# Performance work log

Hardware: AMD Instinct MI355X
Metric: run time of the kernel (lower is better)

The kernel has to match this reference:

```python
import jax, jax.numpy as jnp
import numpy as np

B, T, U = 8192, 1024, 1024  # batch, token_length, units

def _glorot(key, shape):
    fan_in, fan_out = shape
    limit = np.sqrt(6.0 / (fan_in + fan_out))
    return jax.random.uniform(key, shape, jnp.float32, -limit, limit)

def setup_inputs() -> dict:
    key = jax.random.key(0)
    ks = jax.random.split(key, 7)
    x = jax.random.normal(ks[0], (B, T), jnp.float32)
    h = jax.random.normal(ks[1], (B, U), jnp.float32)
    c = jax.random.normal(ks[2], (B, U), jnp.float32)
    W_i = _glorot(ks[3], (T + U, U))
    W_f = _glorot(ks[4], (T + U, U))
    W_g = _glorot(ks[5], (T + U, U))
    W_o = _glorot(ks[6], (T + U, U))
    b_i = jnp.zeros((U,), jnp.float32)
    b_f = jnp.zeros((U,), jnp.float32)
    b_g = jnp.zeros((U,), jnp.float32)
    b_o = jnp.zeros((U,), jnp.float32)
    return {"x": x, "h": h, "c": c, "W_i": W_i, "W_f": W_f, "W_g": W_g,
            "W_o": W_o, "b_i": b_i, "b_f": b_f, "b_g": b_g, "b_o": b_o}

def reference(x, h, c, W_i, W_f, W_g, W_o, b_i, b_f, b_g, b_o):
    x_h = jnp.concatenate([x, h], axis=-1)  # [B, T+U]
    # fused wide GEMM over the four gates
    W = jnp.concatenate([W_i, W_f, W_g, W_o], axis=1)  # [T+U, 4U]
    b = jnp.concatenate([b_i, b_f, b_g, b_o], axis=0)  # [4U]
    z = x_h @ W + b  # [B, 4U]
    zi, zf, zg, zo = jnp.split(z, 4, axis=-1)
    i = jax.nn.sigmoid(zi)
    f = jax.nn.sigmoid(zf)
    g = jnp.tanh(zg)
    o = jax.nn.sigmoid(zo)
    c_new = f * c + i * g
    h_new = o * jnp.tanh(c_new)
    return (h_new, c_new)
```

## Files before the change

### kernel.cpp

```cpp
#include <hip/hip_runtime.h>
#include <hip/hip_bf16.h>
#include <stdint.h>

#define NKT 32
#define BK 64
#define BM 128
#define GCOLS 128

typedef float f32x4 __attribute__((ext_vector_type(4)));
typedef __bf16 bf16x8 __attribute__((ext_vector_type(8)));

static __device__ __forceinline__ void gll16(const void* g, void* l) {
  __builtin_amdgcn_global_load_lds(
      (const __attribute__((address_space(1))) void*)g,
      (__attribute__((address_space(3))) void*)l, 16, 0, 0);
}

static __device__ __forceinline__ unsigned short f2bf(float f) {
  __hip_bfloat16 h = __float2bfloat16(f);
  union { __hip_bfloat16 h; unsigned short u; } v{h};
  return v.u;
}

__global__ void pack_a(const float* __restrict__ x, const float* __restrict__ h,
                       char* __restrict__ Ap) {
  int t   = blockIdx.x * 256 + threadIdx.x;
  int row = t >> 8;
  int cg  = t & 255;
  int kt  = cg >> 3;
  int c   = cg & 7;
  int rb  = row >> 7;
  int r   = row & 127;
  int gk  = kt * 64 + c * 8;
  const float* src = (gk < 1024) ? (x + (size_t)row * 1024 + gk)
                                 : (h + (size_t)row * 1024 + (gk - 1024));
  float4 lo = *(const float4*)(src);
  float4 hi = *(const float4*)(src + 4);
  unsigned short o[8] = { f2bf(lo.x), f2bf(lo.y), f2bf(lo.z), f2bf(lo.w),
                          f2bf(hi.x), f2bf(hi.y), f2bf(hi.z), f2bf(hi.w) };
  size_t tile = ((size_t)rb * NKT + kt) * 16384;
  char* dst = Ap + tile + (size_t)r * 128 + ((c ^ (r & 7)) * 16);
  *(int4*)dst = *(const int4*)o;
}

__global__ void pack_w(const float* __restrict__ Wi, const float* __restrict__ Wf,
                       const float* __restrict__ Wg, const float* __restrict__ Wo,
                       char* __restrict__ Wp) {
  __shared__ float tile[64][33];
  int kt = blockIdx.x, cb = blockIdx.y, g = blockIdx.z;
  const float* W = (g == 0) ? Wi : (g == 1) ? Wf : (g == 2) ? Wg : Wo;
  int t = threadIdx.x;
  {
    int k  = t >> 2;
    int co = (t & 3) * 8;
    const float* s = W + ((size_t)(kt * 64 + k)) * 1024 + cb * 32 + co;
    float4 lo = *(const float4*)s;
    float4 hi = *(const float4*)(s + 4);
    tile[k][co + 0] = lo.x; tile[k][co + 1] = lo.y; tile[k][co + 2] = lo.z; tile[k][co + 3] = lo.w;
    tile[k][co + 4] = hi.x; tile[k][co + 5] = hi.y; tile[k][co + 6] = hi.z; tile[k][co + 7] = hi.w;
  }
  __syncthreads();
  {
    int gcl = t >> 3;
    int cch = t & 7;
    int gc  = g * 32 + gcl;
    unsigned short o[8];
#pragma unroll
    for (int j = 0; j < 8; ++j) o[j] = f2bf(tile[cch * 8 + j][gcl]);
    size_t tb = ((size_t)cb * NKT + kt) * 16384;
    char* dst = Wp + tb + (size_t)gc * 128 + ((cch ^ (gc & 7)) * 16);
    *(int4*)dst = *(const int4*)o;
  }
}

__global__ __launch_bounds__(256, 2)
void lstm_gemm(const char* __restrict__ Ap, const char* __restrict__ Wp,
               const float* __restrict__ c_in,
               const float* __restrict__ b_i, const float* __restrict__ b_f,
               const float* __restrict__ b_g, const float* __restrict__ b_o,
               float* __restrict__ out) {
  __shared__ __align__(128) char smem[32768];
  char* sA = smem;
  char* sB = smem + 16384;

  int cb = blockIdx.x, rb = blockIdx.y;
  int tid = threadIdx.x;
  int w = tid >> 6, lane = tid & 63;
  int l15 = lane & 15, lq = lane >> 4;

  f32x4 acc[2][8] = {};

  const char* aBase = Ap + ((size_t)rb * NKT) * 16384;
  const char* bBase = Wp + ((size_t)cb * NKT) * 16384;

  int rA0 = w * 32 + l15;
  int rA1 = rA0 + 16;
  int aSwz0 = (rA0 & 7) << 4, aSwz1 = (rA1 & 7) << 4;

  for (int kt = 0; kt < NKT; ++kt) {
    const char* at = aBase + (size_t)kt * 16384;
    const char* bt = bBase + (size_t)kt * 16384;
#pragma unroll
    for (int i = 0; i < 4; ++i) {
      int ldso = (i * 4 + w) * 1024;
      int off  = ldso + lane * 16;
      gll16(at + off, sA + ldso);
      gll16(bt + off, sB + ldso);
    }
    __syncthreads();
#pragma unroll
    for (int ks = 0; ks < 2; ++ks) {
      int kterm = ks * 64 + lq * 16;
      bf16x8 a0 = *(const bf16x8*)(sA + rA0 * 128 + (kterm ^ aSwz0));
      bf16x8 a1 = *(const bf16x8*)(sA + rA1 * 128 + (kterm ^ aSwz1));
#pragma unroll
      for (int n = 0; n < 8; ++n) {
        int gc = n * 16 + l15;
        bf16x8 b = *(const bf16x8*)(sB + gc * 128 + (kterm ^ ((gc & 7) << 4)));
        acc[0][n] = __builtin_amdgcn_mfma_f32_16x16x32_bf16(a0, b, acc[0][n], 0, 0, 0);
        acc[1][n] = __builtin_amdgcn_mfma_f32_16x16x32_bf16(a1, b, acc[1][n], 0, 0, 0);
      }
    }
    __syncthreads();
  }

  const size_t HN = (size_t)8192 * 1024;
#pragma unroll
  for (int ci = 0; ci < 2; ++ci) {
    int col = cb * 32 + ci * 16 + l15;
    float bi = b_i[col], bf = b_f[col], bg = b_g[col], bo = b_o[col];
#pragma unroll
    for (int m = 0; m < 2; ++m) {
      f32x4 zi = acc[m][0 + ci], zf = acc[m][2 + ci];
      f32x4 zg = acc[m][4 + ci], zo = acc[m][6 + ci];
      int row0 = rb * 128 + w * 32 + m * 16 + lq * 4;
#pragma unroll
      for (int r = 0; r < 4; ++r) {
        int row = row0 + r;
        float xi = zi[r] + bi, xf = zf[r] + bf, xg = zg[r] + bg, xo = zo[r] + bo;
        float iv = 1.f / (1.f + __expf(-xi));
        float fv = 1.f / (1.f + __expf(-xf));
        float gv = 1.f - 2.f / (__expf(2.f * xg) + 1.f);
        float ov = 1.f / (1.f + __expf(-xo));
        float cv = c_in[(size_t)row * 1024 + col];
        float cn = fv * cv + iv * gv;
        float tc = 1.f - 2.f / (__expf(2.f * cn) + 1.f);
        out[(size_t)row * 1024 + col]      = ov * tc;
        out[HN + (size_t)row * 1024 + col] = cn;
      }
    }
  }
}

extern "C" void kernel_launch(void* const* d_in, const int* in_sizes, int n_in,
                              void* d_out, int out_size, void* d_ws, size_t ws_size,
                              hipStream_t stream) {
  const float* x  = (const float*)d_in[0];
  const float* h  = (const float*)d_in[1];
  const float* c  = (const float*)d_in[2];
  const float* Wi = (const float*)d_in[3];
  const float* Wf = (const float*)d_in[4];
  const float* Wg = (const float*)d_in[5];
  const float* Wo = (const float*)d_in[6];
  const float* bi = (const float*)d_in[7];
  const float* bf = (const float*)d_in[8];
  const float* bg = (const float*)d_in[9];
  const float* bo = (const float*)d_in[10];

  char* Ap = (char*)d_ws;
  char* Wp = Ap + (size_t)8192 * 2048 * 2;
  float* out = (float*)d_out;

  hipLaunchKernelGGL(pack_a, dim3(8192), dim3(256), 0, stream, x, h, Ap);
  hipLaunchKernelGGL(pack_w, dim3(32, 32, 4), dim3(256), 0, stream, Wi, Wf, Wg, Wo, Wp);
  hipLaunchKernelGGL(lstm_gemm, dim3(32, 64), dim3(256), 0, stream,
                     Ap, Wp, c, bi, bf, bg, bo, out);
}
```

Before: 318.9 us.

## Restructure LSTM GEMM into 256x256 tiles with 4-stage async LDS pipeline

Repacks A and W into 32-wide K tiles with a new XOR swizzle, and raises the GEMM block tile to 256x256 with 512 threads (8 waves in a 2x4 grid). It adds a 4-buffer global_load_lds pipeline that prefetches three tiles ahead, interleaved with MFMA bursts under s_setprio, plus a swizzled block-to-tile mapping for L2 locality. The goal is to hide global load latency and raise arithmetic intensity per LDS byte over the old single-buffered 128x128 loop. In exchange it uses 128KB of LDS and many accumulator registers, which limits occupancy, and the manual vmcnt waits are fragile.

```diff
diff --git a/kernel.cpp b/kernel.cpp
--- a/kernel.cpp
+++ b/kernel.cpp
@@ -2,10 +2,6 @@
 #include <hip/hip_bf16.h>
 #include <stdint.h>
 
-#define NKT 32
-#define BK 64
-#define BM 128
-#define GCOLS 128
 
 typedef float f32x4 __attribute__((ext_vector_type(4)));
 typedef __bf16 bf16x8 __attribute__((ext_vector_type(8)));
@@ -17,137 +13,165 @@
 }
 
 static __device__ __forceinline__ unsigned short f2bf(float f) {
-  __hip_bfloat16 h = __float2bfloat16(f);
-  union { __hip_bfloat16 h; unsigned short u; } v{h};
+  union { __hip_bfloat16 h; unsigned short u; } v{__float2bfloat16(f)};
   return v.u;
 }
 
 __global__ void pack_a(const float* __restrict__ x, const float* __restrict__ h,
                        char* __restrict__ Ap) {
-  int t   = blockIdx.x * 256 + threadIdx.x;
-  int row = t >> 8;
-  int cg  = t & 255;
-  int kt  = cg >> 3;
-  int c   = cg & 7;
-  int rb  = row >> 7;
-  int r   = row & 127;
-  int gk  = kt * 64 + c * 8;
+  int row = blockIdx.x;
+  int c8  = threadIdx.x;
+  int kt  = c8 >> 2, kq = c8 & 3;
+  int gk  = c8 * 8;
   const float* src = (gk < 1024) ? (x + (size_t)row * 1024 + gk)
                                  : (h + (size_t)row * 1024 + (gk - 1024));
-  float4 lo = *(const float4*)(src);
+  float4 lo = *(const float4*)src;
   float4 hi = *(const float4*)(src + 4);
-  unsigned short o[8] = { f2bf(lo.x), f2bf(lo.y), f2bf(lo.z), f2bf(lo.w),
-                          f2bf(hi.x), f2bf(hi.y), f2bf(hi.z), f2bf(hi.w) };
-  size_t tile = ((size_t)rb * NKT + kt) * 16384;
-  char* dst = Ap + tile + (size_t)r * 128 + ((c ^ (r & 7)) * 16);
+  __attribute__((aligned(16))) unsigned short o[8] = {
+      f2bf(lo.x), f2bf(lo.y), f2bf(lo.z), f2bf(lo.w),
+      f2bf(hi.x), f2bf(hi.y), f2bf(hi.z), f2bf(hi.w) };
+  int r = row & 255;
+  int chunk = r * 4 + (kq ^ ((r >> 1) & 3));
+  char* dst = Ap + ((size_t)((row >> 8) * 64 + kt)) * 16384 + chunk * 16;
   *(int4*)dst = *(const int4*)o;
 }
 
 __global__ void pack_w(const float* __restrict__ Wi, const float* __restrict__ Wf,
                        const float* __restrict__ Wg, const float* __restrict__ Wo,
                        char* __restrict__ Wp) {
-  __shared__ float tile[64][33];
-  int kt = blockIdx.x, cb = blockIdx.y, g = blockIdx.z;
+  __shared__ float tile[32][65];
+  int kt = blockIdx.x;
+  int cbo = blockIdx.y;
+  int g = blockIdx.z;
   const float* W = (g == 0) ? Wi : (g == 1) ? Wf : (g == 2) ? Wg : Wo;
   int t = threadIdx.x;
   {
-    int k  = t >> 2;
-    int co = (t & 3) * 8;
-    const float* s = W + ((size_t)(kt * 64 + k)) * 1024 + cb * 32 + co;
+    int k  = t >> 3;
+    int c8 = (t & 7) * 8;
+    const float* s = W + (size_t)(kt * 32 + k) * 1024 + cbo * 64 + c8;
     float4 lo = *(const float4*)s;
     float4 hi = *(const float4*)(s + 4);
-    tile[k][co + 0] = lo.x; tile[k][co + 1] = lo.y; tile[k][co + 2] = lo.z; tile[k][co + 3] = lo.w;
-    tile[k][co + 4] = hi.x; tile[k][co + 5] = hi.y; tile[k][co + 6] = hi.z; tile[k][co + 7] = hi.w;
+    tile[k][c8 + 0] = lo.x; tile[k][c8 + 1] = lo.y; tile[k][c8 + 2] = lo.z; tile[k][c8 + 3] = lo.w;
+    tile[k][c8 + 4] = hi.x; tile[k][c8 + 5] = hi.y; tile[k][c8 + 6] = hi.z; tile[k][c8 + 7] = hi.w;
   }
   __syncthreads();
   {
-    int gcl = t >> 3;
-    int cch = t & 7;
-    int gc  = g * 32 + gcl;
-    unsigned short o[8];
-#pragma unroll
-    for (int j = 0; j < 8; ++j) o[j] = f2bf(tile[cch * 8 + j][gcl]);
-    size_t tb = ((size_t)cb * NKT + kt) * 16384;
-    char* dst = Wp + tb + (size_t)gc * 128 + ((cch ^ (gc & 7)) * 16);
+    int cl = t >> 2;
+    int kq = t & 3;
+    __attribute__((aligned(16))) unsigned short o[8];
+#pragma unroll
+    for (int j = 0; j < 8; ++j) o[j] = f2bf(tile[kq * 8 + j][cl]);
+    int gc = ((cl >> 4) & 3) * 64 + g * 16 + (cl & 15);
+    int chunk = gc * 4 + (kq ^ ((gc >> 1) & 3));
+    char* dst = Wp + ((size_t)(cbo * 64 + kt)) * 16384 + chunk * 16;
     *(int4*)dst = *(const int4*)o;
   }
 }
 
-__global__ __launch_bounds__(256, 2)
+__global__ __launch_bounds__(512, 2)
 void lstm_gemm(const char* __restrict__ Ap, const char* __restrict__ Wp,
                const float* __restrict__ c_in,
                const float* __restrict__ b_i, const float* __restrict__ b_f,
                const float* __restrict__ b_g, const float* __restrict__ b_o,
                float* __restrict__ out) {
-  __shared__ __align__(128) char smem[32768];
-  char* sA = smem;
-  char* sB = smem + 16384;
-
-  int cb = blockIdx.x, rb = blockIdx.y;
+  __shared__ __align__(128) char smem[131072];
+
   int tid = threadIdx.x;
-  int w = tid >> 6, lane = tid & 63;
-  int l15 = lane & 15, lq = lane >> 4;
-
-  f32x4 acc[2][8] = {};
-
-  const char* aBase = Ap + ((size_t)rb * NKT) * 16384;
-  const char* bBase = Wp + ((size_t)cb * NKT) * 16384;
-
-  int rA0 = w * 32 + l15;
-  int rA1 = rA0 + 16;
-  int aSwz0 = (rA0 & 7) << 4, aSwz1 = (rA1 & 7) << 4;
-
-  for (int kt = 0; kt < NKT; ++kt) {
-    const char* at = aBase + (size_t)kt * 16384;
-    const char* bt = bBase + (size_t)kt * 16384;
-#pragma unroll
-    for (int i = 0; i < 4; ++i) {
-      int ldso = (i * 4 + w) * 1024;
-      int off  = ldso + lane * 16;
-      gll16(at + off, sA + ldso);
-      gll16(bt + off, sB + ldso);
-    }
-    __syncthreads();
-#pragma unroll
-    for (int ks = 0; ks < 2; ++ks) {
-      int kterm = ks * 64 + lq * 16;
-      bf16x8 a0 = *(const bf16x8*)(sA + rA0 * 128 + (kterm ^ aSwz0));
-      bf16x8 a1 = *(const bf16x8*)(sA + rA1 * 128 + (kterm ^ aSwz1));
-#pragma unroll
-      for (int n = 0; n < 8; ++n) {
-        int gc = n * 16 + l15;
-        bf16x8 b = *(const bf16x8*)(sB + gc * 128 + (kterm ^ ((gc & 7) << 4)));
-        acc[0][n] = __builtin_amdgcn_mfma_f32_16x16x32_bf16(a0, b, acc[0][n], 0, 0, 0);
-        acc[1][n] = __builtin_amdgcn_mfma_f32_16x16x32_bf16(a1, b, acc[1][n], 0, 0, 0);
-      }
-    }
-    __syncthreads();
-  }
-
+  int w = tid >> 6, lane = tid & 63, l15 = lane & 15, lq = lane >> 4;
+  int wm = w >> 2, wc = w & 3;
+
+  int bid = blockIdx.x;
+  int wg = (bid & 7) * 64 + (bid >> 3);
+  int rbB = wg >> 4, cb = wg & 15;
+
+  const char* aT = Ap + (size_t)rbB * (64 * 16384);
+  const char* bT = Wp + (size_t)cb * (64 * 16384);
+
+  f32x4 acc[8][4] = {};
+
+  int aOff[8], bOff[4];
+#pragma unroll
+  for (int m = 0; m < 8; ++m) {
+    int r = wm * 128 + m * 16 + l15;
+    aOff[m] = r * 64 + ((lq ^ ((r >> 1) & 3)) << 4);
+  }
+#pragma unroll
+  for (int n = 0; n < 4; ++n) {
+    int gc = wc * 64 + n * 16 + l15;
+    bOff[n] = gc * 64 + ((lq ^ ((gc >> 1) & 3)) << 4);
+  }
+
+  auto stgA = [&](int kt) {
+    const char* s = aT + (size_t)kt * 16384 + tid * 16;
+    char* d = smem + (kt & 3) * 32768 + tid * 16;
+    gll16(s, d); gll16(s + 8192, d + 8192);
+  };
+  auto stgB = [&](int kt) {
+    const char* s = bT + (size_t)kt * 16384 + tid * 16;
+    char* d = smem + (kt & 3) * 32768 + 16384 + tid * 16;
+    gll16(s, d); gll16(s + 8192, d + 8192);
+  };
+
+  stgA(0); stgB(0); stgA(1); stgB(1); stgA(2); stgB(2);
+  asm volatile("s_waitcnt vmcnt(8)" ::: "memory");
+  __builtin_amdgcn_s_barrier();
+
+  for (int j = 0; j < 64; ++j) {
+    const char* sA = smem + (j & 3) * 32768;
+    const char* sB = sA + 16384;
+    int js = (j + 3) & 63;
+
+    bf16x8 aF[4], bF[4], aG[4];
+#pragma unroll
+    for (int m = 0; m < 4; ++m) aF[m] = *(const bf16x8*)(sA + aOff[m]);
+#pragma unroll
+    for (int n = 0; n < 4; ++n) bF[n] = *(const bf16x8*)(sB + bOff[n]);
+    stgA(js);
+    __builtin_amdgcn_s_barrier();
+    __builtin_amdgcn_s_setprio(1);
+#pragma unroll
+    for (int m = 0; m < 4; ++m)
+#pragma unroll
+      for (int n = 0; n < 4; ++n)
+        acc[m][n] = __builtin_amdgcn_mfma_f32_16x16x32_bf16(aF[m], bF[n], acc[m][n], 0, 0, 0);
+    __builtin_amdgcn_s_setprio(0);
+    __builtin_amdgcn_s_barrier();
+
+#pragma unroll
+    for (int m = 0; m < 4; ++m) aG[m] = *(const bf16x8*)(sA + aOff[4 + m]);
+    stgB(js);
+    __builtin_amdgcn_s_barrier();
+    __builtin_amdgcn_s_setprio(1);
+#pragma unroll
+    for (int m = 0; m < 4; ++m)
+#pragma unroll
+      for (int n = 0; n < 4; ++n)
+        acc[4 + m][n] = __builtin_amdgcn_mfma_f32_16x16x32_bf16(aG[m], bF[n], acc[4 + m][n], 0, 0, 0);
+    __builtin_amdgcn_s_setprio(0);
+    asm volatile("s_waitcnt vmcnt(8)" ::: "memory");
+    __builtin_amdgcn_s_barrier();
+  }
+
+  int col = (cb * 4 + wc) * 16 + l15;
+  float Bi = b_i[col], Bf = b_f[col], Bg = b_g[col], Bo = b_o[col];
   const size_t HN = (size_t)8192 * 1024;
 #pragma unroll
-  for (int ci = 0; ci < 2; ++ci) {
-    int col = cb * 32 + ci * 16 + l15;
-    float bi = b_i[col], bf = b_f[col], bg = b_g[col], bo = b_o[col];
-#pragma unroll
-    for (int m = 0; m < 2; ++m) {
-      f32x4 zi = acc[m][0 + ci], zf = acc[m][2 + ci];
-      f32x4 zg = acc[m][4 + ci], zo = acc[m][6 + ci];
-      int row0 = rb * 128 + w * 32 + m * 16 + lq * 4;
-#pragma unroll
-      for (int r = 0; r < 4; ++r) {
-        int row = row0 + r;
-        float xi = zi[r] + bi, xf = zf[r] + bf, xg = zg[r] + bg, xo = zo[r] + bo;
-        float iv = 1.f / (1.f + __expf(-xi));
-        float fv = 1.f / (1.f + __expf(-xf));
-        float gv = 1.f - 2.f / (__expf(2.f * xg) + 1.f);
-        float ov = 1.f / (1.f + __expf(-xo));
-        float cv = c_in[(size_t)row * 1024 + col];
-        float cn = fv * cv + iv * gv;
-        float tc = 1.f - 2.f / (__expf(2.f * cn) + 1.f);
-        out[(size_t)row * 1024 + col]      = ov * tc;
-        out[HN + (size_t)row * 1024 + col] = cn;
-      }
+  for (int mf = 0; mf < 8; ++mf) {
+    int row0 = rbB * 256 + wm * 128 + mf * 16 + lq * 4;
+#pragma unroll
+    for (int r = 0; r < 4; ++r) {
+      int row = row0 + r;
+      float xi = acc[mf][0][r] + Bi, xf = acc[mf][1][r] + Bf;
+      float xg = acc[mf][2][r] + Bg, xo = acc[mf][3][r] + Bo;
+      float iv = 1.f / (1.f + __expf(-xi));
+      float fv = 1.f / (1.f + __expf(-xf));
+      float gv = 1.f - 2.f / (__expf(2.f * xg) + 1.f);
+      float ov = 1.f / (1.f + __expf(-xo));
+      float cv = c_in[(size_t)row * 1024 + col];
+      float cn = fv * cv + iv * gv;
+      float tc = 1.f - 2.f / (__expf(2.f * cn) + 1.f);
+      out[(size_t)row * 1024 + col]      = ov * tc;
+      out[HN + (size_t)row * 1024 + col] = cn;
     }
   }
 }
@@ -172,7 +196,7 @@
   float* out = (float*)d_out;
 
   hipLaunchKernelGGL(pack_a, dim3(8192), dim3(256), 0, stream, x, h, Ap);
-  hipLaunchKernelGGL(pack_w, dim3(32, 32, 4), dim3(256), 0, stream, Wi, Wf, Wg, Wo, Wp);
-  hipLaunchKernelGGL(lstm_gemm, dim3(32, 64), dim3(256), 0, stream,
+  hipLaunchKernelGGL(pack_w, dim3(64, 16, 4), dim3(256), 0, stream, Wi, Wf, Wg, Wo, Wp);
+  hipLaunchKernelGGL(lstm_gemm, dim3(512), dim3(512), 0, stream,
                      Ap, Wp, c, bi, bf, bg, bo, out);
 }
```

Result: no change. 313.3 us (-1.7%).
